# Optimization experiments

Hardware: AMD Instinct MI355X
Metric: run time of the kernel (lower is better)

## Reference

```python
import jax, jax.numpy as jnp
import numpy as np

NEG_SLOPE = 0.2  # PyG GATConv default LeakyReLU slope


def gat_layer(x, edge_index, W, att_src, att_dst, bias, concat, num_nodes):
    """PyG GATConv (add_self_loops=False, dropout=0, bias=True).
    x: [N, in], W: [in, H*C], att_src/att_dst: [H, C], bias: [H*C] or [C].
    """
    H, C = att_src.shape
    h = (x @ W).reshape(num_nodes, H, C)                      # [N, H, C]
    src, dst = edge_index[0], edge_index[1]                   # messages src -> dst
    a_src = jnp.sum(h * att_src[None], axis=-1)               # [N, H]
    a_dst = jnp.sum(h * att_dst[None], axis=-1)               # [N, H]
    e = jax.nn.leaky_relu(a_src[src] + a_dst[dst], NEG_SLOPE)  # [E, H]
    # segment softmax over edges sharing the same dst node
    e_max = jax.ops.segment_max(e, dst, num_segments=num_nodes)
    e_max = jnp.where(jnp.isfinite(e_max), e_max, 0.0)
    ex = jnp.exp(e - e_max[dst])
    denom = jax.ops.segment_sum(ex, dst, num_segments=num_nodes)
    alpha = ex / (denom[dst] + 1e-16)                          # [E, H]
    msg = h[src] * alpha[:, :, None]                           # [E, H, C]
    out = jax.ops.segment_sum(msg, dst, num_segments=num_nodes)  # [N, H, C]
    out = out.reshape(num_nodes, H * C) if concat else out.mean(axis=1)
    return out + bias


def setup_inputs() -> dict:
    key = jax.random.key(0)
    ks = jax.random.split(key, 12)
    NU, NI, D, H, C = 40000, 40000, 64, 2, 64
    N = NU + NI
    E = 1_280_000
    B = 8192
    s = 0.05
    return {
        "Gu": jax.random.normal(ks[0], (NU, D), jnp.float32) * s,
        "Gi": jax.random.normal(ks[1], (NI, D), jnp.float32) * s,
        "W0": jax.random.normal(ks[2], (D, H * C), jnp.float32) * s,
        "att_src0": jax.random.normal(ks[3], (H, C), jnp.float32) * s,
        "att_dst0": jax.random.normal(ks[4], (H, C), jnp.float32) * s,
        "b0": jnp.zeros((H * C,), jnp.float32),
        "W1": jax.random.normal(ks[5], (H * C, H * C), jnp.float32) * s,
        "att_src1": jax.random.normal(ks[6], (H, C), jnp.float32) * s,
        "att_dst1": jax.random.normal(ks[7], (H, C), jnp.float32) * s,
        "b1": jnp.zeros((C,), jnp.float32),
        "edge_index": jax.random.randint(ks[8], (2, E), 0, N, jnp.int32),
        "user_idx": jax.random.randint(ks[9], (B,), 0, NU, jnp.int32),
        "item_idx": jax.random.randint(ks[10], (B,), 0, NI, jnp.int32),
    }


def reference(Gu, Gi, W0, att_src0, att_dst0, b0, W1, att_src1, att_dst1, b1,
              edge_index, user_idx, item_idx):
    num_users = Gu.shape[0]
    x = jnp.concatenate([Gu, Gi], axis=0)
    N = x.shape[0]
    # layer 0: concat=True, layer 1 (final): concat=False (mean over heads)
    x = gat_layer(x, edge_index, W0, att_src0, att_dst0, b0, True, N)
    x = gat_layer(x, edge_index, W1, att_src1, att_dst1, b1, False, N)
    gu, gi = x[:num_users], x[num_users:]
    # forward(): rowwise dot product of user/item embeddings
    xui = jnp.sum(gu[user_idx] * gi[item_idx], axis=1)
    return xui
```

## Files before the change

### kernel.cpp

```cpp
#include <hip/hip_runtime.h>
#include <hip/hip_fp16.h>
#include <math.h>

#define N_NODES   80000
#define NU_NODES  40000
#define E_EDGES   1280000
#define B_PAIRS   8192
#define NEG_SLOPE 0.2f
#define NBUCK     313
#define SCHUNK    2048

typedef _Float16 half8 __attribute__((ext_vector_type(8)));
typedef float    f32x4 __attribute__((ext_vector_type(4)));


__global__ __launch_bounds__(512) void bhist313_kernel(const int* __restrict__ dst,
                                                       int* __restrict__ bucketCount, int E) {
    __shared__ int histL[NBUCK];
    for (int i = threadIdx.x; i < NBUCK; i += 512) histL[i] = 0;
    __syncthreads();
    int base = blockIdx.x * SCHUNK;
#pragma unroll
    for (int r = 0; r < SCHUNK / 512; ++r) {
        int e = base + r * 512 + threadIdx.x;
        if (e < E) atomicAdd(&histL[dst[e] >> 8], 1);
    }
    __syncthreads();
    for (int i = threadIdx.x; i < NBUCK; i += 512)
        if (histL[i]) atomicAdd(&bucketCount[i], histL[i]);
}

__global__ __launch_bounds__(512) void topscan_kernel(const int* __restrict__ bucketCount,
                                                      int* __restrict__ bucket_ptr,
                                                      int* __restrict__ gfill) {
    __shared__ int tmp[512];
    int t = threadIdx.x;
    int v = (t < NBUCK) ? bucketCount[t] : 0;
    tmp[t] = v;
    __syncthreads();
    for (int off = 1; off < 512; off <<= 1) {
        int x = (t >= off) ? tmp[t - off] : 0;
        __syncthreads();
        tmp[t] += x;
        __syncthreads();
    }
    int excl = tmp[t] - v;
    if (t < NBUCK) {
        bucket_ptr[t] = excl;
        gfill[t]      = excl;
        if (t == NBUCK - 1) bucket_ptr[NBUCK] = excl + v;
    }
}

__global__ __launch_bounds__(512) void bscatter_kernel(const int* __restrict__ src,
                                                       const int* __restrict__ dst,
                                                       int* __restrict__ gfill,
                                                       unsigned long long* __restrict__ pk,
                                                       int E) {
    __shared__ int histL[NBUCK];
    __shared__ int baseL[NBUCK];
    __shared__ int rankL[NBUCK];
    for (int i = threadIdx.x; i < NBUCK; i += 512) { histL[i] = 0; rankL[i] = 0; }
    __syncthreads();
    int base = blockIdx.x * SCHUNK;
#pragma unroll
    for (int r = 0; r < SCHUNK / 512; ++r) {
        int e = base + r * 512 + threadIdx.x;
        if (e < E) atomicAdd(&histL[dst[e] >> 8], 1);
    }
    __syncthreads();
    for (int i = threadIdx.x; i < NBUCK; i += 512)
        baseL[i] = histL[i] ? atomicAdd(&gfill[i], histL[i]) : 0;
    __syncthreads();
#pragma unroll
    for (int r = 0; r < SCHUNK / 512; ++r) {
        int e = base + r * 512 + threadIdx.x;
        if (e < E) {
            int d = dst[e];
            int b = d >> 8;
            int rk = atomicAdd(&rankL[b], 1);
            pk[baseL[b] + rk] = ((unsigned long long)(unsigned)d << 32) | (unsigned)src[e];
        }
    }
}

__global__ __launch_bounds__(256) void escatter2_kernel(
        const unsigned long long* __restrict__ pk, const int* __restrict__ bucket_ptr,
        int* __restrict__ row_ptr, int* __restrict__ src_sorted) {
    __shared__ int cntL[256];
    __shared__ int tmp[256];
    __shared__ int rpL[256];
    int b = blockIdx.x;
    int t = threadIdx.x;
    int node0 = b << 8;
    int s = bucket_ptr[b], e = bucket_ptr[b + 1];
    cntL[t] = 0;
    __syncthreads();
    for (int k = s + t; k < e; k += 256) atomicAdd(&cntL[(int)(pk[k] >> 32) & 255], 1);
    __syncthreads();
    int v = cntL[t];
    tmp[t] = v;
    __syncthreads();
    for (int off = 1; off < 256; off <<= 1) {
        int x = (t >= off) ? tmp[t - off] : 0;
        __syncthreads();
        tmp[t] += x;
        __syncthreads();
    }
    int excl = tmp[t] - v;
    rpL[t] = s + excl;
    int node = node0 + t;
    if (node < N_NODES) row_ptr[node] = s + excl;
    if (b == NBUCK - 1 && t == 0) row_ptr[N_NODES] = e;
    cntL[t] = 0;
    __syncthreads();
    for (int k = s + t; k < e; k += 256) {
        unsigned long long p = pk[k];
        int lo = (int)(p >> 32) & 255;
        int pos = atomicAdd(&cntL[lo], 1);
        src_sorted[rpL[lo] + pos] = (int)(unsigned)p;
    }
}


template <int K, bool AF32>
__global__ __launch_bounds__(256) void gemm_mfma(const void* __restrict__ A0v,
                                                 const void* __restrict__ A1v, int split,
                                                 const float* __restrict__ W,
                                                 const float* __restrict__ attS,
                                                 const float* __restrict__ attD,
                                                 __half* __restrict__ hh,
                                                 float* __restrict__ a_s,
                                                 float* __restrict__ a_d) {
    constexpr int BSTR   = K + 8;
    constexpr int BSM_SZ = 128 * BSTR * 2;
    constexpr int EPI_SZ = 128 * 136 * 2;
    constexpr int ATT_OFF = (10240 + BSM_SZ > EPI_SZ) ? (10240 + BSM_SZ) : EPI_SZ;
    __shared__ __align__(16) char lds[ATT_OFF + 1024];
    _Float16* Asm  = (_Float16*)lds;
    _Float16* Bsm  = (_Float16*)(lds + 10240);
    _Float16* epi  = (_Float16*)lds;
    float*    attL = (float*)(lds + ATT_OFF);

    const int tid    = threadIdx.x;
    const int w      = tid >> 6;
    const int l      = tid & 63;
    const int l15    = l & 15;
    const int g      = l >> 4;
    const int blkrow = blockIdx.x * 128;

    attL[tid] = (tid < 128) ? attS[tid] : attD[tid - 128];

    for (int idx = tid; idx < K * 32; idx += 256) {
        int k = idx >> 5, c4 = idx & 31;
        float4 wv = *(const float4*)&W[(size_t)k * 128 + c4 * 4];
        Bsm[(c4 * 4 + 0) * BSTR + k] = (_Float16)wv.x;
        Bsm[(c4 * 4 + 1) * BSTR + k] = (_Float16)wv.y;
        Bsm[(c4 * 4 + 2) * BSTR + k] = (_Float16)wv.z;
        Bsm[(c4 * 4 + 3) * BSTR + k] = (_Float16)wv.w;
    }

    const void* rowp[2];
#pragma unroll
    for (int p = 0; p < 2; ++p) {
        int idx = tid + p * 256;
        int row = idx >> 2;
        int grow = blkrow + row;
        if (AF32) {
            const float* A0 = (const float*)A0v;
            const float* A1 = (const float*)A1v;
            rowp[p] = (grow < split) ? (const void*)(A0 + (size_t)grow * K)
                                     : (const void*)(A1 + (size_t)(grow - split) * K);
        } else {
            rowp[p] = (const void*)((const _Float16*)A0v + (size_t)grow * K);
        }
    }

    auto stageA = [&](int c) {
#pragma unroll
        for (int p = 0; p < 2; ++p) {
            int idx = tid + p * 256;
            int row = idx >> 2, kq = idx & 3;
            half8 hv;
            if (AF32) {
                const float* ap = (const float*)rowp[p];
                float4 v0 = *(const float4*)&ap[c * 32 + kq * 8];
                float4 v1 = *(const float4*)&ap[c * 32 + kq * 8 + 4];
                hv[0] = (_Float16)v0.x; hv[1] = (_Float16)v0.y;
                hv[2] = (_Float16)v0.z; hv[3] = (_Float16)v0.w;
                hv[4] = (_Float16)v1.x; hv[5] = (_Float16)v1.y;
                hv[6] = (_Float16)v1.z; hv[7] = (_Float16)v1.w;
            } else {
                const _Float16* ap = (const _Float16*)rowp[p];
                hv = *(const half8*)&ap[c * 32 + kq * 8];
            }
            *(half8*)&Asm[row * 40 + kq * 8] = hv;
        }
    };

    f32x4 acc[2][8];
#pragma unroll
    for (int rt = 0; rt < 2; ++rt)
#pragma unroll
        for (int ct = 0; ct < 8; ++ct) acc[rt][ct] = (f32x4){0.f, 0.f, 0.f, 0.f};

    constexpr int CH = K / 32;
    stageA(0);
    __syncthreads();
#pragma unroll
    for (int c = 0; c < CH; ++c) {
        half8 a0 = *(const half8*)&Asm[(w * 32 + l15) * 40 + g * 8];
        half8 a1 = *(const half8*)&Asm[(w * 32 + 16 + l15) * 40 + g * 8];
#pragma unroll
        for (int ct = 0; ct < 8; ++ct) {
            half8 b = *(const half8*)&Bsm[(ct * 16 + l15) * BSTR + c * 32 + g * 8];
            acc[0][ct] = __builtin_amdgcn_mfma_f32_16x16x32_f16(a0, b, acc[0][ct], 0, 0, 0);
            acc[1][ct] = __builtin_amdgcn_mfma_f32_16x16x32_f16(a1, b, acc[1][ct], 0, 0, 0);
        }
        __syncthreads();
        if (c + 1 < CH) {
            stageA(c + 1);
            __syncthreads();
        }
    }

#pragma unroll
    for (int rt = 0; rt < 2; ++rt)
#pragma unroll
        for (int reg = 0; reg < 4; ++reg) {
            float s0 = 0.f, s1 = 0.f, d0 = 0.f, d1 = 0.f;
#pragma unroll
            for (int ct = 0; ct < 4; ++ct) {
                float v = acc[rt][ct][reg];
                s0 = fmaf(v, attL[ct * 16 + l15], s0);
                d0 = fmaf(v, attL[128 + ct * 16 + l15], d0);
            }
#pragma unroll
            for (int ct = 4; ct < 8; ++ct) {
                float v = acc[rt][ct][reg];
                s1 = fmaf(v, attL[ct * 16 + l15], s1);
                d1 = fmaf(v, attL[128 + ct * 16 + l15], d1);
            }
#pragma unroll
            for (int o = 1; o < 16; o <<= 1) {
                s0 += __shfl_xor(s0, o); s1 += __shfl_xor(s1, o);
                d0 += __shfl_xor(d0, o); d1 += __shfl_xor(d1, o);
            }
            if (l15 == 0) {
                int row = blkrow + w * 32 + rt * 16 + g * 4 + reg;
                *(float2*)&a_s[row * 2] = make_float2(s0, s1);
                *(float2*)&a_d[row * 2] = make_float2(d0, d1);
            }
        }

#pragma unroll
    for (int rt = 0; rt < 2; ++rt)
#pragma unroll
        for (int ct = 0; ct < 8; ++ct)
#pragma unroll
            for (int reg = 0; reg < 4; ++reg)
                epi[(w * 32 + rt * 16 + g * 4 + reg) * 136 + ct * 16 + l15] =
                    (_Float16)acc[rt][ct][reg];
    __syncthreads();
#pragma unroll
    for (int p = 0; p < 8; ++p) {
        int idx = tid + p * 256;
        int row = idx >> 4, c8 = idx & 15;
        *(half8*)&hh[(size_t)(blkrow + row) * 128 + c8 * 8] =
            *(const half8*)&epi[row * 136 + c8 * 8];
    }
}


template <bool CONCAT>
__global__ __launch_bounds__(256) void gat_agg_kernel(const __half* __restrict__ hh,
        const int* __restrict__ row_ptr, const int* __restrict__ src_sorted,
        const float* __restrict__ a_s, const float* __restrict__ a_d,
        const float* __restrict__ bias, void* __restrict__ outv) {
    __shared__ int   s_idx[4][64];
    __shared__ float s_w[4][64][2];
    int wid   = threadIdx.x >> 6;
    int lane  = threadIdx.x & 63;
    int dnode = blockIdx.x * 4 + wid;
    if (dnode >= N_NODES) return;
    int start = row_ptr[dnode], end = row_ptr[dnode + 1];
    int deg = end - start;
    float2 ad = *(const float2*)(a_d + dnode * 2);
    int hh_head = lane >> 5;
    float2 acc = {0.f, 0.f};
    float den0 = 0.f, den1 = 0.f;
    const __half2* h2 = (const __half2*)hh;

    if (deg <= 64) {
        if (lane < deg) {
            int s = src_sorted[start + lane];
            float2 as = *(const float2*)(a_s + s * 2);
            float v0 = as.x + ad.x; v0 = v0 > 0.f ? v0 : NEG_SLOPE * v0;
            float v1 = as.y + ad.y; v1 = v1 > 0.f ? v1 : NEG_SLOPE * v1;
            float w0 = __expf(v0), w1 = __expf(v1);
            den0 = w0; den1 = w1;
            s_idx[wid][lane] = s;
            s_w[wid][lane][0] = w0;
            s_w[wid][lane][1] = w1;
        }
        for (int o = 32; o; o >>= 1) {
            den0 += __shfl_xor(den0, o);
            den1 += __shfl_xor(den1, o);
        }
        int j = 0;
#pragma unroll 1
        for (; j + 4 <= deg; j += 4) {
            int   si0 = s_idx[wid][j + 0], si1 = s_idx[wid][j + 1];
            int   si2 = s_idx[wid][j + 2], si3 = s_idx[wid][j + 3];
            float w0 = s_w[wid][j + 0][hh_head], w1 = s_w[wid][j + 1][hh_head];
            float w2 = s_w[wid][j + 2][hh_head], w3 = s_w[wid][j + 3][hh_head];
            float2 q0 = __half22float2(h2[(size_t)si0 * 64 + lane]);
            float2 q1 = __half22float2(h2[(size_t)si1 * 64 + lane]);
            float2 q2 = __half22float2(h2[(size_t)si2 * 64 + lane]);
            float2 q3 = __half22float2(h2[(size_t)si3 * 64 + lane]);
            acc.x = fmaf(w0, q0.x, acc.x); acc.y = fmaf(w0, q0.y, acc.y);
            acc.x = fmaf(w1, q1.x, acc.x); acc.y = fmaf(w1, q1.y, acc.y);
            acc.x = fmaf(w2, q2.x, acc.x); acc.y = fmaf(w2, q2.y, acc.y);
            acc.x = fmaf(w3, q3.x, acc.x); acc.y = fmaf(w3, q3.y, acc.y);
        }
        for (; j < deg; ++j) {
            int  si = s_idx[wid][j];
            float w = s_w[wid][j][hh_head];
            float2 v = __half22float2(h2[(size_t)si * 64 + lane]);
            acc.x = fmaf(w, v.x, acc.x);
            acc.y = fmaf(w, v.y, acc.y);
        }
    } else {
        for (int c0 = start; c0 < end; c0 += 64) {
            int len = min(64, end - c0);
            if (lane < len) {
                int s = src_sorted[c0 + lane];
                float2 as = *(const float2*)(a_s + s * 2);
                float v0 = as.x + ad.x; v0 = v0 > 0.f ? v0 : NEG_SLOPE * v0;
                float v1 = as.y + ad.y; v1 = v1 > 0.f ? v1 : NEG_SLOPE * v1;
                float w0 = __expf(v0), w1 = __expf(v1);
                den0 += w0; den1 += w1;
                s_idx[wid][lane] = s;
                s_w[wid][lane][0] = w0;
                s_w[wid][lane][1] = w1;
            }
            for (int j = 0; j < len; ++j) {
                int  si = s_idx[wid][j];
                float w = s_w[wid][j][hh_head];
                float2 v = __half22float2(h2[(size_t)si * 64 + lane]);
                acc.x = fmaf(w, v.x, acc.x);
                acc.y = fmaf(w, v.y, acc.y);
            }
        }
        for (int o = 32; o; o >>= 1) {
            den0 += __shfl_xor(den0, o);
            den1 += __shfl_xor(den1, o);
        }
    }

    float inv = 1.f / ((hh_head ? den1 : den0) + 1e-16f);
    float2 r = {acc.x * inv, acc.y * inv};

    if (CONCAT) {
        __half* out = (__half*)outv;
        float2 b = *(const float2*)(bias + lane * 2);
        __half2 o2 = __floats2half2_rn(r.x + b.x, r.y + b.y);
        *(__half2*)(out + (size_t)dnode * 128 + lane * 2) = o2;
    } else {
        float* out = (float*)outv;
        float ox = __shfl_xor(r.x, 32);
        float oy = __shfl_xor(r.y, 32);
        if (lane < 32) {
            float2 b = *(const float2*)(bias + lane * 2);
            float2 o2 = {0.5f * (r.x + ox) + b.x, 0.5f * (r.y + oy) + b.y};
            *(float2*)(out + (size_t)dnode * 64 + lane * 2) = o2;
        }
    }
}


__global__ void pair_dot_kernel(const float* __restrict__ emb, const int* __restrict__ ui,
                                const int* __restrict__ ii, float* __restrict__ out, int B) {
    int w    = blockIdx.x * 4 + (threadIdx.x >> 6);
    int lane = threadIdx.x & 63;
    if (w >= B) return;
    float a = emb[(size_t)ui[w] * 64 + lane];
    float b = emb[(size_t)(NU_NODES + ii[w]) * 64 + lane];
    float p = a * b;
    for (int o = 32; o; o >>= 1) p += __shfl_xor(p, o);
    if (lane == 0) out[w] = p;
}

extern "C" void kernel_launch(void* const* d_in, const int* in_sizes, int n_in,
                              void* d_out, int out_size, void* d_ws, size_t ws_size,
                              hipStream_t stream) {
    const float* Gu       = (const float*)d_in[0];
    const float* Gi       = (const float*)d_in[1];
    const float* W0       = (const float*)d_in[2];
    const float* att_src0 = (const float*)d_in[3];
    const float* att_dst0 = (const float*)d_in[4];
    const float* b0       = (const float*)d_in[5];
    const float* W1       = (const float*)d_in[6];
    const float* att_src1 = (const float*)d_in[7];
    const float* att_dst1 = (const float*)d_in[8];
    const float* b1       = (const float*)d_in[9];
    const int* edge_index = (const int*)d_in[10];
    const int* user_idx   = (const int*)d_in[11];
    const int* item_idx   = (const int*)d_in[12];
    float* outp           = (float*)d_out;

    const int N = N_NODES, E = E_EDGES;
    char* wsp = (char*)d_ws;
    auto alloc = [&](size_t bytes) {
        void* p = wsp;
        wsp += (bytes + 255) & ~(size_t)255;
        return p;
    };
    float*  emb = (float*)alloc((size_t)N * 64 * 4);
    __half* hh  = (__half*)alloc((size_t)N * 128 * 2);
    __half* x1h = (__half*)alloc((size_t)N * 128 * 2);
    float*  a_s = (float*)alloc((size_t)N * 2 * 4);
    float*  a_d = (float*)alloc((size_t)N * 2 * 4);
    int* row_ptr     = (int*)alloc((size_t)(N + 1) * 4);
    int* src_sorted  = (int*)alloc((size_t)E * 4);
    int* bucketCount = (int*)alloc((NBUCK + 1) * 4);
    int* bucket_ptr  = (int*)alloc((NBUCK + 1) * 4);
    int* gfill       = (int*)alloc((NBUCK + 1) * 4);
    unsigned long long* pk = (unsigned long long*)x1h;

    const int* esrc = edge_index;
    const int* edst = edge_index + E;

    hipMemsetAsync(bucketCount, 0, (NBUCK + 1) * 4, stream);
    int nblk = (E + SCHUNK - 1) / SCHUNK;
    bhist313_kernel<<<nblk, 512, 0, stream>>>(edst, bucketCount, E);
    topscan_kernel<<<1, 512, 0, stream>>>(bucketCount, bucket_ptr, gfill);
    bscatter_kernel<<<nblk, 512, 0, stream>>>(esrc, edst, gfill, pk, E);
    escatter2_kernel<<<NBUCK, 256, 0, stream>>>(pk, bucket_ptr, row_ptr, src_sorted);

    gemm_mfma<64, true><<<N / 128, 256, 0, stream>>>(Gu, Gi, NU_NODES, W0, att_src0, att_dst0,
                                                     hh, a_s, a_d);
    gat_agg_kernel<true><<<(N + 3) / 4, 256, 0, stream>>>(hh, row_ptr, src_sorted, a_s, a_d,
                                                          b0, x1h);

    gemm_mfma<128, false><<<N / 128, 256, 0, stream>>>(x1h, x1h, N, W1, att_src1, att_dst1,
                                                       hh, a_s, a_d);
    gat_agg_kernel<false><<<(N + 3) / 4, 256, 0, stream>>>(hh, row_ptr, src_sorted, a_s, a_d,
                                                           b1, emb);

    pair_dot_kernel<<<B_PAIRS / 4, 256, 0, stream>>>(emb, user_idx, item_idx, outp, B_PAIRS);
}
```

Baseline: 224.5 us.

## Fuse dst-bucket histogram into first GEMM and prefetch A tiles into registers

```diff
diff --git a/kernel.cpp b/kernel.cpp
--- a/kernel.cpp
+++ b/kernel.cpp
@@ -13,22 +13,6 @@
 typedef _Float16 half8 __attribute__((ext_vector_type(8)));
 typedef float    f32x4 __attribute__((ext_vector_type(4)));
 
-
-__global__ __launch_bounds__(512) void bhist313_kernel(const int* __restrict__ dst,
-                                                       int* __restrict__ bucketCount, int E) {
-    __shared__ int histL[NBUCK];
-    for (int i = threadIdx.x; i < NBUCK; i += 512) histL[i] = 0;
-    __syncthreads();
-    int base = blockIdx.x * SCHUNK;
-#pragma unroll
-    for (int r = 0; r < SCHUNK / 512; ++r) {
-        int e = base + r * 512 + threadIdx.x;
-        if (e < E) atomicAdd(&histL[dst[e] >> 8], 1);
-    }
-    __syncthreads();
-    for (int i = threadIdx.x; i < NBUCK; i += 512)
-        if (histL[i]) atomicAdd(&bucketCount[i], histL[i]);
-}
 
 __global__ __launch_bounds__(512) void topscan_kernel(const int* __restrict__ bucketCount,
                                                       int* __restrict__ bucket_ptr,
@@ -123,7 +107,7 @@
 }
 
 
-template <int K, bool AF32>
+template <int K, bool AF32, bool HIST>
 __global__ __launch_bounds__(256) void gemm_mfma(const void* __restrict__ A0v,
                                                  const void* __restrict__ A1v, int split,
                                                  const float* __restrict__ W,
@@ -131,16 +115,19 @@
                                                  const float* __restrict__ attD,
                                                  __half* __restrict__ hh,
                                                  float* __restrict__ a_s,
-                                                 float* __restrict__ a_d) {
+                                                 float* __restrict__ a_d,
+                                                 const int* __restrict__ edst,
+                                                 int* __restrict__ bucketCount) {
     constexpr int BSTR   = K + 8;
     constexpr int BSM_SZ = 128 * BSTR * 2;
     constexpr int EPI_SZ = 128 * 136 * 2;
     constexpr int ATT_OFF = (10240 + BSM_SZ > EPI_SZ) ? (10240 + BSM_SZ) : EPI_SZ;
-    __shared__ __align__(16) char lds[ATT_OFF + 1024];
+    __shared__ __align__(16) char lds[ATT_OFF + 1024 + (HIST ? (NBUCK + 7) * 4 : 4)];
     _Float16* Asm  = (_Float16*)lds;
     _Float16* Bsm  = (_Float16*)(lds + 10240);
     _Float16* epi  = (_Float16*)lds;
     float*    attL = (float*)(lds + ATT_OFF);
+    int*      histL = (int*)(lds + ATT_OFF + 1024);
 
     const int tid    = threadIdx.x;
     const int w      = tid >> 6;
@@ -148,6 +135,18 @@
     const int l15    = l & 15;
     const int g      = l >> 4;
     const int blkrow = blockIdx.x * 128;
+
+    if (HIST) {
+        for (int i = tid; i < NBUCK; i += 256) histL[i] = 0;
+        __syncthreads();
+        int base = blockIdx.x * SCHUNK;
+#pragma unroll
+        for (int r = 0; r < SCHUNK / 256; ++r)
+            atomicAdd(&histL[edst[base + r * 256 + tid] >> 8], 1);
+        __syncthreads();
+        for (int i = tid; i < NBUCK; i += 256)
+            if (histL[i]) atomicAdd(&bucketCount[i], histL[i]);
+    }
 
     attL[tid] = (tid < 128) ? attS[tid] : attD[tid - 128];
 
@@ -176,27 +175,33 @@
         }
     }
 
-    auto stageA = [&](int c) {
+    auto loadA = [&](int c, half8* hv) {
 #pragma unroll
         for (int p = 0; p < 2; ++p) {
             int idx = tid + p * 256;
-            int row = idx >> 2, kq = idx & 3;
-            half8 hv;
+            int kq = idx & 3;
             if (AF32) {
                 const float* ap = (const float*)rowp[p];
                 float4 v0 = *(const float4*)&ap[c * 32 + kq * 8];
                 float4 v1 = *(const float4*)&ap[c * 32 + kq * 8 + 4];
-                hv[0] = (_Float16)v0.x; hv[1] = (_Float16)v0.y;
-                hv[2] = (_Float16)v0.z; hv[3] = (_Float16)v0.w;
-                hv[4] = (_Float16)v1.x; hv[5] = (_Float16)v1.y;
-                hv[6] = (_Float16)v1.z; hv[7] = (_Float16)v1.w;
+                hv[p][0] = (_Float16)v0.x; hv[p][1] = (_Float16)v0.y;
+                hv[p][2] = (_Float16)v0.z; hv[p][3] = (_Float16)v0.w;
+                hv[p][4] = (_Float16)v1.x; hv[p][5] = (_Float16)v1.y;
+                hv[p][6] = (_Float16)v1.z; hv[p][7] = (_Float16)v1.w;
             } else {
                 const _Float16* ap = (const _Float16*)rowp[p];
-                hv = *(const half8*)&ap[c * 32 + kq * 8];
-            }
-            *(half8*)&Asm[row * 40 + kq * 8] = hv;
+                hv[p] = *(const half8*)&ap[c * 32 + kq * 8];
+            }
         }
     };
+    auto writeA = [&](half8* hv) {
+#pragma unroll
+        for (int p = 0; p < 2; ++p) {
+            int idx = tid + p * 256;
+            int row = idx >> 2, kq = idx & 3;
+            *(half8*)&Asm[row * 40 + kq * 8] = hv[p];
+        }
+    };
 
     f32x4 acc[2][8];
 #pragma unroll
@@ -205,10 +210,13 @@
         for (int ct = 0; ct < 8; ++ct) acc[rt][ct] = (f32x4){0.f, 0.f, 0.f, 0.f};
 
     constexpr int CH = K / 32;
-    stageA(0);
+    half8 cur[2], nxt[2];
+    loadA(0, cur);
+    writeA(cur);
     __syncthreads();
 #pragma unroll
     for (int c = 0; c < CH; ++c) {
+        if (c + 1 < CH) loadA(c + 1, nxt);
         half8 a0 = *(const half8*)&Asm[(w * 32 + l15) * 40 + g * 8];
         half8 a1 = *(const half8*)&Asm[(w * 32 + 16 + l15) * 40 + g * 8];
 #pragma unroll
@@ -219,7 +227,7 @@
         }
         __syncthreads();
         if (c + 1 < CH) {
-            stageA(c + 1);
+            writeA(nxt);
             __syncthreads();
         }
     }
@@ -432,19 +440,20 @@
     const int* edst = edge_index + E;
 
     hipMemsetAsync(bucketCount, 0, (NBUCK + 1) * 4, stream);
+
+    gemm_mfma<64, true, true><<<N / 128, 256, 0, stream>>>(
+        Gu, Gi, NU_NODES, W0, att_src0, att_dst0, hh, a_s, a_d, edst, bucketCount);
+
+    topscan_kernel<<<1, 512, 0, stream>>>(bucketCount, bucket_ptr, gfill);
     int nblk = (E + SCHUNK - 1) / SCHUNK;
-    bhist313_kernel<<<nblk, 512, 0, stream>>>(edst, bucketCount, E);
-    topscan_kernel<<<1, 512, 0, stream>>>(bucketCount, bucket_ptr, gfill);
     bscatter_kernel<<<nblk, 512, 0, stream>>>(esrc, edst, gfill, pk, E);
     escatter2_kernel<<<NBUCK, 256, 0, stream>>>(pk, bucket_ptr, row_ptr, src_sorted);
 
-    gemm_mfma<64, true><<<N / 128, 256, 0, stream>>>(Gu, Gi, NU_NODES, W0, att_src0, att_dst0,
-                                                     hh, a_s, a_d);
     gat_agg_kernel<true><<<(N + 3) / 4, 256, 0, stream>>>(hh, row_ptr, src_sorted, a_s, a_d,
                                                           b0, x1h);
 
-    gemm_mfma<128, false><<<N / 128, 256, 0, stream>>>(x1h, x1h, N, W1, att_src1, att_dst1,
-                                                       hh, a_s, a_d);
+    gemm_mfma<128, false, false><<<N / 128, 256, 0, stream>>>(
+        x1h, x1h, N, W1, att_src1, att_dst1, hh, a_s, a_d, nullptr, nullptr);
     gat_agg_kernel<false><<<(N + 3) / 4, 256, 0, stream>>>(hh, row_ptr, src_sorted, a_s, a_d,
                                                            b1, emb);
 
```

New measurement: 222.4 us. Within noise of the previous version (-1.0%).
